# Performance work log

Measured on AMD Instinct MI355X. Metric: run time of the kernel, lower is better.

The kernel has to match this reference:

```python
import jax, jax.numpy as jnp
import numpy as np

B, T, I, H, O = 32, 128, 256, 256, 128

def setup_inputs() -> dict:
    key = jax.random.key(0)
    k = jax.random.split(key, 7)
    init_k = 1.0 / np.sqrt(H)
    sentence = jax.random.normal(k[0], (B, T, I), dtype=jnp.float32)
    weight_lambda = jax.random.uniform(k[1], (H, H + I), minval=0.0, maxval=1.0, dtype=jnp.float32)
    weight_gamma = jax.random.uniform(k[2], (H, H + I), minval=-0.001 * init_k, maxval=0.001 * init_k, dtype=jnp.float32)
    weight = jax.random.uniform(k[3], (H, H + I), minval=-init_k, maxval=init_k, dtype=jnp.float32)
    bias = jax.random.uniform(k[4], (H,), minval=-init_k, maxval=init_k, dtype=jnp.float32)
    W_out = jax.random.uniform(k[5], (O, H), minval=-init_k, maxval=init_k, dtype=jnp.float32)
    b_out = jax.random.uniform(k[6], (O,), minval=-init_k, maxval=init_k, dtype=jnp.float32)
    return {"sentence": sentence, "weight_lambda": weight_lambda, "weight_gamma": weight_gamma,
            "weight": weight, "bias": bias, "W_out": W_out, "b_out": b_out}

def reference(sentence, weight_lambda, weight_gamma, weight, bias, W_out, b_out):
    b = sentence.shape[0]
    h0 = jnp.zeros((b, H), dtype=sentence.dtype)
    F0 = jnp.zeros((b, H, H + I), dtype=sentence.dtype)

    def step(carry, x_t):
        h, F = carry
        total_input = jnp.concatenate([x_t, h], axis=1)           # (B, I+H)
        total_weights = weight + F                                 # (B, H, I+H)
        h_new = jnp.tanh(jnp.einsum('bf,bhf->bh', total_input, total_weights) + bias)
        norm = jnp.linalg.norm(total_weights, axis=2, keepdims=True) + 1e-16  # (B, H, 1)
        h_new = h_new / norm[..., 0]
        F_new = weight_lambda * (F / norm) + weight_gamma * jnp.einsum('bf,bh->bhf', total_input, h_new)
        return (h_new, F_new), None

    (h_T, F_T), _ = jax.lax.scan(step, (h0, F0), jnp.swapaxes(sentence, 0, 1))
    tag_space = h_T @ W_out.T + b_out
    return tag_space, h_T, F_T
```

## Files before the change

kernel.cpp:

```cpp
#include <hip/hip_runtime.h>

#define BB 32
#define TT 128
#define II 256
#define HH 256
#define OO 128
#define FWID 512
#define FAST_TIMEOUT 128


typedef unsigned long long u64;
typedef float f32x2 __attribute__((ext_vector_type(2)));

__device__ __forceinline__ f32x2 mk2(float a, float b) { f32x2 r; r.x = a; r.y = b; return r; }

__device__ __forceinline__ f32x2 pk_fma(f32x2 a, f32x2 b, f32x2 c) {
    f32x2 d;
    asm("v_pk_fma_f32 %0, %1, %2, %3" : "=v"(d) : "v"(a), "v"(b), "v"(c));
    return d;
}
__device__ __forceinline__ f32x2 pk_mul(f32x2 a, f32x2 b) {
    f32x2 d;
    asm("v_pk_mul_f32 %0, %1, %2" : "=v"(d) : "v"(a), "v"(b));
    return d;
}
__device__ __forceinline__ f32x2 pk_add(f32x2 a, f32x2 b) {
    f32x2 d;
    asm("v_pk_add_f32 %0, %1, %2" : "=v"(d) : "v"(a), "v"(b));
    return d;
}

template<int CTRL>
__device__ __forceinline__ float dpp_add(float x) {
    int t = __builtin_amdgcn_update_dpp(0, __float_as_int(x), CTRL, 0xF, 0xF, true);
    return x + __int_as_float(t);
}
__device__ __forceinline__ float row16_sum(float x) {
    x = dpp_add<0x128>(x);
    x = dpp_add<0x124>(x);
    x = dpp_add<0x122>(x);
    x = dpp_add<0x121>(x);
    return x;
}

__device__ __forceinline__ u64 slot_ld(const u64* p) {
    return __hip_atomic_load(p, __ATOMIC_RELAXED, __HIP_MEMORY_SCOPE_AGENT);
}

__device__ __forceinline__ void fast_load4(const u64* p, u64& a, u64& b, u64& c, u64& d) {
    asm volatile(
        "global_load_dwordx2 %0, %4, off sc0\n\t"
        "global_load_dwordx2 %1, %4, off offset:8 sc0\n\t"
        "global_load_dwordx2 %2, %4, off offset:16 sc0\n\t"
        "global_load_dwordx2 %3, %4, off offset:24 sc0\n\t"
        "s_waitcnt vmcnt(0)"
        : "=&v"(a), "=&v"(b), "=&v"(c), "=&v"(d)
        : "v"(p)
        : "memory");
}

__device__ __forceinline__ void gather_to_lds(const u64* sbase, const u64* fbase,
                                              int lane, unsigned us,
                                              float* dst, int* flag, int fval,
                                              bool& fellback) {
    u64 a, b, c, d;
    bool got = false;
    if (fbase && !fellback) {
        const u64* pf = fbase + 4 * lane;
        int spins = 0;
        for (;;) {
            fast_load4(pf, a, b, c, d);
            bool ok = ((unsigned)(a >> 32) >= us) & ((unsigned)(b >> 32) >= us) &
                      ((unsigned)(c >> 32) >= us) & ((unsigned)(d >> 32) >= us);
            if (__all(ok)) { got = true; break; }
            if (++spins > FAST_TIMEOUT) break;
        }
        if (!got) fellback = true;
    }
    if (!got) {
        const u64* p = sbase + 4 * lane;
        for (;;) {
            a = slot_ld(p);
            b = slot_ld(p + 1);
            c = slot_ld(p + 2);
            d = slot_ld(p + 3);
            bool ok = ((unsigned)(a >> 32) >= us) & ((unsigned)(b >> 32) >= us) &
                      ((unsigned)(c >> 32) >= us) & ((unsigned)(d >> 32) >= us);
            if (__all(ok)) break;
        }
    }
    float4 hv;
    hv.x = __uint_as_float((unsigned)a);
    hv.y = __uint_as_float((unsigned)b);
    hv.z = __uint_as_float((unsigned)c);
    hv.w = __uint_as_float((unsigned)d);
    *reinterpret_cast<float4*>(dst + 4 * lane) = hv;
    if (lane == 0)
        __hip_atomic_store(flag, fval, __ATOMIC_RELEASE, __HIP_MEMORY_SCOPE_WORKGROUP);
}

__global__ __launch_bounds__(512, 2)
void stpn_kernel(const float* __restrict__ x,
                 const float* __restrict__ wlam,
                 const float* __restrict__ wgam,
                 const float* __restrict__ w,
                 const float* __restrict__ bias,
                 const float* __restrict__ wout,
                 const float* __restrict__ bout,
                 float* __restrict__ out,
                 u64* __restrict__ slots,
                 u64* __restrict__ fasts)
{
    __shared__ __align__(16) float lh[2][HH];
    __shared__ int lflag[2];

    const int tid  = threadIdx.x;
    const int bk   = blockIdx.x;
    const int b    = bk & 31;
    const int sl   = bk >> 5;
    const int wv   = tid >> 6;
    const int lane = tid & 63;
    const int g    = tid >> 4;
    const int i    = tid & 15;
    const int r    = sl * 32 + (g & 31);

    if (tid < 2) lflag[tid] = 0;
    bool fellback = false;
    const bool have_fast = (fasts != nullptr);

    f32x2 W2[16], Lm2[16], G2[16], F2[16];
    {
        const float4* wr = reinterpret_cast<const float4*>(w    + (size_t)r * FWID);
        const float4* lr = reinterpret_cast<const float4*>(wlam + (size_t)r * FWID);
        const float4* gr = reinterpret_cast<const float4*>(wgam + (size_t)r * FWID);
#pragma unroll
        for (int k = 0; k < 8; ++k) {
            float4 t;
            t = wr[k * 16 + i]; W2[2*k]  = mk2(t.x, t.y); W2[2*k+1]  = mk2(t.z, t.w);
            t = lr[k * 16 + i]; Lm2[2*k] = mk2(t.x, t.y); Lm2[2*k+1] = mk2(t.z, t.w);
            t = gr[k * 16 + i]; G2[2*k]  = mk2(t.x, t.y); G2[2*k+1]  = mk2(t.z, t.w);
            F2[2*k] = mk2(0.f, 0.f); F2[2*k+1] = mk2(0.f, 0.f);
        }
    }
    const float bj = bias[r];
    float hl = 0.f;

    float4 px0, px1, px2, px3;
    {
        const float4* xb4 = reinterpret_cast<const float4*>(x + (size_t)b * TT * II);
        px0 = xb4[i]; px1 = xb4[16 + i]; px2 = xb4[32 + i]; px3 = xb4[48 + i];
    }

    __syncthreads();

    for (int s = 0; s < TT; ++s) {
        const int par = s & 1;

        f32x2 X2[8];
        X2[0] = mk2(px0.x, px0.y); X2[1] = mk2(px0.z, px0.w);
        X2[2] = mk2(px1.x, px1.y); X2[3] = mk2(px1.z, px1.w);
        X2[4] = mk2(px2.x, px2.y); X2[5] = mk2(px2.z, px2.w);
        X2[6] = mk2(px3.x, px3.y); X2[7] = mk2(px3.z, px3.w);

        f32x2 tw2[8];
        f32x2 dx2 = mk2(0.f, 0.f), nv2 = mk2(0.f, 0.f);
#pragma unroll
        for (int j = 0; j < 8; ++j) {
            f32x2 t = pk_add(W2[j], F2[j]);
            dx2 = pk_fma(X2[j], t, dx2);
            nv2 = pk_fma(t, t, nv2);
        }
#pragma unroll
        for (int j = 0; j < 8; ++j) {
            tw2[j] = pk_add(W2[8 + j], F2[8 + j]);
            nv2 = pk_fma(tw2[j], tw2[j], nv2);
        }
        float dxs = dx2.x + dx2.y;
        float nrm = nv2.x + nv2.y;
        dxs = row16_sum(dxs);
        nrm = row16_sum(nrm);
        const float invn = __builtin_amdgcn_rsqf(nrm);
        const f32x2 invn2 = mk2(invn, invn);
        const float dxb = dxs + bj;

#pragma unroll
        for (int j = 0; j < 16; ++j) F2[j] = pk_mul(Lm2[j], pk_mul(F2[j], invn2));

        if (wv == 0) {
            gather_to_lds(slots + ((size_t)par * BB + b) * HH,
                          have_fast ? fasts + ((size_t)par * BB + b) * HH : nullptr,
                          lane, (unsigned)s, lh[par], &lflag[par], s + 1, fellback);
        }

        while (__hip_atomic_load(&lflag[par], __ATOMIC_ACQUIRE, __HIP_MEMORY_SCOPE_WORKGROUP) <= s) {}
        const float4* lh4 = reinterpret_cast<const float4*>(lh[par]);
        float4 ha = lh4[i], hb = lh4[16 + i], hc = lh4[32 + i], hd = lh4[48 + i];
        f32x2 H2[8];
        H2[0] = mk2(ha.x, ha.y); H2[1] = mk2(ha.z, ha.w);
        H2[2] = mk2(hb.x, hb.y); H2[3] = mk2(hb.z, hb.w);
        H2[4] = mk2(hc.x, hc.y); H2[5] = mk2(hc.z, hc.w);
        H2[6] = mk2(hd.x, hd.y); H2[7] = mk2(hd.z, hd.w);

        f32x2 a2 = pk_mul(H2[0], tw2[0]);
        f32x2 b2 = pk_mul(H2[1], tw2[1]);
        a2 = pk_fma(H2[2], tw2[2], a2);
        b2 = pk_fma(H2[3], tw2[3], b2);
        a2 = pk_fma(H2[4], tw2[4], a2);
        b2 = pk_fma(H2[5], tw2[5], b2);
        a2 = pk_fma(H2[6], tw2[6], a2);
        b2 = pk_fma(H2[7], tw2[7], b2);
        f32x2 c2 = pk_add(a2, b2);
        float dh = c2.x + c2.y;
        dh = row16_sum(dh);

        const float e = __expf(2.0f * (dxb + dh));
        const float h = (1.0f - 2.0f * __builtin_amdgcn_rcpf(e + 1.0f)) * invn;
        hl = h;

        if (i == 0) {
            const u64 val = ((u64)(unsigned)(s + 1) << 32) | (unsigned)__float_as_uint(h);
            const size_t idx = ((size_t)(par ^ 1) * BB + b) * HH + r;
            if (have_fast) {
                u64* pf = fasts + idx;
                asm volatile("global_store_dwordx2 %0, %1, off sc0" :: "v"(pf), "v"(val) : "memory");
            }
            __hip_atomic_store(slots + idx, val, __ATOMIC_RELAXED, __HIP_MEMORY_SCOPE_AGENT);
        }

        if (s + 1 < TT) {
            const float4* xn = reinterpret_cast<const float4*>(x + ((size_t)b * TT + (s + 1)) * II);
            px0 = xn[i]; px1 = xn[16 + i]; px2 = xn[32 + i]; px3 = xn[48 + i];
        }

        const f32x2 h2v = mk2(h, h);
#pragma unroll
        for (int j = 0; j < 8; ++j)
            F2[j] = pk_fma(pk_mul(X2[j], G2[j]), h2v, F2[j]);
#pragma unroll
        for (int j = 0; j < 8; ++j)
            F2[8 + j] = pk_fma(pk_mul(G2[8 + j], H2[j]), h2v, F2[8 + j]);
    }

    {
        float4* fo = reinterpret_cast<float4*>(out + 12288 + ((size_t)b * HH + r) * FWID);
#pragma unroll
        for (int k = 0; k < 8; ++k) {
            float4 v;
            v.x = F2[2*k].x; v.y = F2[2*k].y; v.z = F2[2*k+1].x; v.w = F2[2*k+1].y;
            fo[k * 16 + i] = v;
        }
    }
    if (i == 0) out[4096 + (size_t)b * HH + r] = hl;

    if (sl == 0) {
        if (wv == 0) {
            gather_to_lds(slots + ((size_t)(TT & 1) * BB + b) * HH,
                          have_fast ? fasts + ((size_t)(TT & 1) * BB + b) * HH : nullptr,
                          lane, (unsigned)TT, lh[0], &lflag[0], TT + 1, fellback);
        }
        while (__hip_atomic_load(&lflag[0], __ATOMIC_ACQUIRE, __HIP_MEMORY_SCOPE_WORKGROUP) <= TT) {}
        if (tid < OO) {
            const float* hv = lh[0];
            float acc = bout[tid];
            const float* wo = wout + (size_t)tid * HH;
#pragma unroll 4
            for (int jj = 0; jj < HH; ++jj) acc = fmaf(wo[jj], hv[jj], acc);
            out[(size_t)b * OO + tid] = acc;
        }
    }
}

extern "C" void kernel_launch(void* const* d_in, const int* in_sizes, int n_in,
                              void* d_out, int out_size, void* d_ws, size_t ws_size,
                              hipStream_t stream) {
    (void)in_sizes; (void)n_in; (void)out_size;
    const float* x    = (const float*)d_in[0];
    const float* wlam = (const float*)d_in[1];
    const float* wgam = (const float*)d_in[2];
    const float* w    = (const float*)d_in[3];
    const float* bias = (const float*)d_in[4];
    const float* wout = (const float*)d_in[5];
    const float* bout = (const float*)d_in[6];
    float* out = (float*)d_out;

    const size_t SLOT_BYTES = 2ull * BB * HH * 8ull;
    u64* slots = (u64*)d_ws;
    u64* fasts = nullptr;
    if (ws_size >= 2 * SLOT_BYTES) {
        fasts = slots + 2ull * BB * HH;
        hipMemsetAsync(d_ws, 0, 2 * SLOT_BYTES, stream);
    } else {
        hipMemsetAsync(d_ws, 0, SLOT_BYTES, stream);
    }

    hipLaunchKernelGGL(stpn_kernel, dim3(256), dim3(512), 0, stream,
                       x, wlam, wgam, w, bias, wout, bout, out, slots, fasts);
}
```

Measured before the change: 258.5 us.

## Assign batch/slice roles by XCC id so each batch's blocks share one XCD

Each block reads its hardware XCC id and takes a per-XCC rank from an atomic counter, then picks its batch and hidden-slice role so that all eight slices of a batch sit on the same XCD. The intent is to keep the cross-block hidden-state exchange inside one XCD's L2, which makes the fast path cheaper. Blocks that overflow an XCC's quota wait for every block to register, take the leftover roles, and have the fast path disabled. This adds an atomic-based startup phase with a spin wait, and relies on all 256 blocks being co-resident.

```diff
diff --git a/kernel.cpp b/kernel.cpp
--- a/kernel.cpp
+++ b/kernel.cpp
@@ -109,24 +109,63 @@
                  const float* __restrict__ bout,
                  float* __restrict__ out,
                  u64* __restrict__ slots,
-                 u64* __restrict__ fasts)
+                 u64* __restrict__ fasts,
+                 unsigned* __restrict__ meta)
 {
     __shared__ __align__(16) float lh[2][HH];
     __shared__ int lflag[2];
+    __shared__ int role_s[3];
 
     const int tid  = threadIdx.x;
     const int bk   = blockIdx.x;
-    const int b    = bk & 31;
-    const int sl   = bk >> 5;
     const int wv   = tid >> 6;
     const int lane = tid & 63;
     const int g    = tid >> 4;
     const int i    = tid & 15;
-    const int r    = sl * 32 + (g & 31);
-
+
+    if (tid == 0) {
+        int b_, sl_, fok = 1;
+        if (meta != nullptr) {
+            unsigned xcc;
+            asm volatile("s_getreg_b32 %0, hwreg(HW_REG_XCC_ID)" : "=s"(xcc));
+            xcc &= 7;
+            unsigned rank = __hip_atomic_fetch_add(&meta[xcc], 1u,
+                                __ATOMIC_RELAXED, __HIP_MEMORY_SCOPE_AGENT);
+            __hip_atomic_fetch_add(&meta[8], 1u,
+                                __ATOMIC_RELEASE, __HIP_MEMORY_SCOPE_AGENT);
+            if (rank < 32u) {
+                b_ = (int)(xcc * 4u + (rank >> 3));
+                sl_ = (int)(rank & 7u);
+            } else {
+                unsigned j = __hip_atomic_fetch_add(&meta[9], 1u,
+                                __ATOMIC_RELAXED, __HIP_MEMORY_SCOPE_AGENT);
+                while (__hip_atomic_load(&meta[8], __ATOMIC_ACQUIRE,
+                                         __HIP_MEMORY_SCOPE_AGENT) < 256u) {}
+                unsigned cnt = 0; b_ = 0; sl_ = 0;
+                for (int xc = 0; xc < 8; ++xc) {
+                    unsigned c = __hip_atomic_load(&meta[xc], __ATOMIC_RELAXED,
+                                                   __HIP_MEMORY_SCOPE_AGENT);
+                    if (c > 32u) c = 32u;
+                    for (unsigned rk = c; rk < 32u; ++rk) {
+                        if (cnt == j) { b_ = (int)(xc * 4 + (rk >> 3)); sl_ = (int)(rk & 7u); }
+                        ++cnt;
+                    }
+                }
+                fok = 0;
+            }
+        } else {
+            b_ = bk & 31; sl_ = bk >> 5; fok = 0;
+        }
+        role_s[0] = b_; role_s[1] = sl_; role_s[2] = fok;
+    }
     if (tid < 2) lflag[tid] = 0;
+    __syncthreads();
+
+    const int b  = role_s[0];
+    const int sl = role_s[1];
+    const bool have_fast = (role_s[2] != 0) && (fasts != nullptr);
+    const int r  = sl * 32 + (g & 31);
     bool fellback = false;
-    const bool have_fast = (fasts != nullptr);
 
     f32x2 W2[16], Lm2[16], G2[16], F2[16];
     {
@@ -150,8 +189,6 @@
         const float4* xb4 = reinterpret_cast<const float4*>(x + (size_t)b * TT * II);
         px0 = xb4[i]; px1 = xb4[16 + i]; px2 = xb4[32 + i]; px3 = xb4[48 + i];
     }
-
-    __syncthreads();
 
     for (int s = 0; s < TT; ++s) {
         const int par = s & 1;
@@ -286,13 +323,15 @@
     const size_t SLOT_BYTES = 2ull * BB * HH * 8ull;
     u64* slots = (u64*)d_ws;
     u64* fasts = nullptr;
-    if (ws_size >= 2 * SLOT_BYTES) {
+    unsigned* meta = nullptr;
+    if (ws_size >= 2 * SLOT_BYTES + 128) {
         fasts = slots + 2ull * BB * HH;
-        hipMemsetAsync(d_ws, 0, 2 * SLOT_BYTES, stream);
+        meta  = (unsigned*)((char*)d_ws + 2 * SLOT_BYTES);
+        hipMemsetAsync(d_ws, 0, 2 * SLOT_BYTES + 128, stream);
     } else {
         hipMemsetAsync(d_ws, 0, SLOT_BYTES, stream);
     }
 
     hipLaunchKernelGGL(stpn_kernel, dim3(256), dim3(512), 0, stream,
-                       x, wlam, wgam, w, bias, wout, bout, out, slots, fasts);
-}
+                       x, wlam, wgam, w, bias, wout, bout, out, slots, fasts, meta);
+}
```

After: 264.6 us. +2.4%, slower.
